# Performance work log

Measured on AMD Instinct MI355X. Metric: run time of the kernel, lower is better.

Reference implementation:

```python
import jax, jax.numpy as jnp
import numpy as np

N_NODES = 4096
JACOBI_ITERS = 10
EPS = 1e-5


def sym_laplacian_dense(edge_index, n):
    # L = I - D^{-1/2} A D^{-1/2}, duplicates in edge_index accumulate (as scipy COO does)
    row, col = edge_index[0], edge_index[1]
    A = jnp.zeros((n, n), jnp.float32).at[row, col].add(1.0)
    deg = A.sum(axis=1)
    dinv = jnp.where(deg > 0, 1.0 / jnp.sqrt(jnp.where(deg > 0, deg, 1.0)), 0.0)
    return jnp.eye(n, dtype=jnp.float32) - dinv[:, None] * A * dinv[None, :]


def jacobi_eig(a, iterations):
    # Faithful Jacobi: `iterations` Givens rotations, each zeroing the max |off-diag| entry.
    n = a.shape[0]
    upper = jnp.triu(jnp.ones((n, n), bool), k=1)

    def body(_, carry):
        a, p = carry
        idx = jnp.argmax(jnp.where(upper, jnp.abs(a), 0.0))
        k, l = idx // n, idx % n
        akl = a[k, l]
        aDiff = a[l, l] - a[k, k]
        akl_safe = jnp.where(akl == 0.0, 1.0, akl)
        aDiff_safe = jnp.where(aDiff == 0.0, 1.0, aDiff)
        phi = aDiff / (2.0 * akl_safe)
        t2 = 1.0 / (jnp.abs(phi) + jnp.sqrt(phi * phi + 1.0))
        t2 = jnp.where(phi < 0.0, -t2, t2)
        t1 = akl / aDiff_safe
        t = jnp.where(jnp.abs(akl) < jnp.abs(aDiff) * 1e-36, t1, t2)
        c = 1.0 / jnp.sqrt(t * t + 1.0)
        s = t * c
        # a <- G^T a G  (equivalent to the triangular in-place updates for symmetric a)
        ck, cl = a[:, k], a[:, l]
        a = a.at[:, k].set(c * ck - s * cl).at[:, l].set(s * ck + c * cl)
        rk, rl = a[k, :], a[l, :]
        a = a.at[k, :].set(c * rk - s * rl).at[l, :].set(s * rk + c * rl)
        a = a.at[k, l].set(0.0).at[l, k].set(0.0)
        pk, pl = p[:, k], p[:, l]
        p = p.at[:, k].set(c * pk - s * pl).at[:, l].set(s * pk + c * pl)
        return a, p

    a, p = jax.lax.fori_loop(0, iterations, body, (a, jnp.eye(n, dtype=a.dtype)))
    return jnp.diagonal(a), p


def setup_inputs() -> dict:
    key = jax.random.key(0)
    ks = jax.random.split(key, 8)
    n, cin, cout, r, e = N_NODES, 64, 64, 4, 100000
    x = jax.random.normal(ks[0], (n, cin), jnp.float32)
    src = jax.random.randint(ks[1], (e,), 0, n)
    dst = jax.random.randint(ks[2], (e,), 0, n)
    # symmetric graph (undirected), as the Jacobi solver assumes a symmetric Laplacian
    edge_index = jnp.stack([jnp.concatenate([src, dst]), jnp.concatenate([dst, src])]).astype(jnp.int64)
    stdv = 1.0 / np.sqrt(cin)
    real_weight = jax.random.uniform(ks[3], (cout, cin, r, 1), jnp.float32, -stdv, stdv)
    imag_weight = jax.random.uniform(ks[4], (cout, cin, r, 1), jnp.float32, -stdv, stdv)
    h = jax.random.uniform(ks[5], (cout, cin), jnp.float32, -stdv, stdv)
    c = jax.random.uniform(ks[6], (cout, cin, 1), jnp.float32, -stdv, stdv)
    bias = jnp.zeros((cout,), jnp.float32)
    return {"x": x, "edge_index": edge_index, "real_weight": real_weight,
            "imag_weight": imag_weight, "h": h, "c": c, "bias": bias}


def reference(x, edge_index, real_weight, imag_weight, h, c, bias):
    n = x.shape[0]
    r = real_weight.shape[2]
    L = sym_laplacian_dense(edge_index, n)
    w, U = jacobi_eig(L, JACOBI_ITERS)          # w: (N,), U: (N, N)
    aux = U.T @ x                                # (N, in)
    hw = h[:, :, None] * w[None, None, :]        # (out, in, N)
    a2 = jnp.where(hw > EPS,
                   2.0 * jnp.arctan(1.0 / jnp.where(hw > EPS, hw, 1.0)),
                   2.0)
    # theta[o,i,j,n] = a2[o,i,n] * (j+1)  -> (out, in, r, N)
    theta = a2[:, :, None, :] * jnp.arange(1, r + 1, dtype=x.dtype)[None, None, :, None]
    g = real_weight * jnp.cos(theta) - imag_weight * jnp.sin(theta)
    g = g.sum(axis=2) + c                        # (out, in, N)
    out = jnp.einsum('oin,ni->on', g, aux)       # Pmul + sum over in-channels
    output = U @ out.T + bias                    # (N, out); note: original's clamp(min=0) is a no-op
    return output
```

## Files before the change

kernel.cpp:

```cpp
#include <hip/hip_runtime.h>
#include <hip/hip_bf16.h>

#pragma clang fp contract(off)

#define N 4096
#define CIN 64
#define COUT 64
#define ITERS 10
#define MAXS 32
#define CANDMAX 384

typedef unsigned long long u64;

__device__ __forceinline__ u64 packkey(float v, unsigned j) {
    return ((u64)__float_as_uint(v) << 32) | (u64)(~j);
}
__device__ __forceinline__ u64 gkey(unsigned vb, unsigned row, unsigned col) {
    unsigned flat = (row << 12) | col;
    return ((u64)vb << 24) | (u64)((~flat) & 0xFFFFFFu);
}

__global__ void init_prep_k(int* __restrict__ deg, int* __restrict__ fill,
                            const float* __restrict__ hh, const float* __restrict__ cw,
                            const float* __restrict__ rw, const float* __restrict__ iw,
                            float2* __restrict__ hcT, float4* __restrict__ rwT,
                            float4* __restrict__ iwT) {
    int b = blockIdx.x;
    if (b < 16) {
        int i = b * 256 + threadIdx.x;
        deg[i] = 0; fill[i] = 0;
    } else {
        int idx = (b - 16) * 256 + threadIdx.x;
        int i = idx >> 6, o = idx & 63;
        int src = o * 64 + i;
        hcT[idx] = make_float2(hh[src], cw[src]);
        rwT[idx] = make_float4(rw[src * 4 + 0], rw[src * 4 + 1], rw[src * 4 + 2], rw[src * 4 + 3]);
        iwT[idx] = make_float4(iw[src * 4 + 0], iw[src * 4 + 1], iw[src * 4 + 2], iw[src * 4 + 3]);
    }
}

__global__ void edges1_k(const int* __restrict__ ei, int* __restrict__ deg, int E) {
    int e = blockIdx.x * 256 + threadIdx.x;
    if (e < E) atomicAdd(&deg[ei[e]], 1);
}

__global__ void __launch_bounds__(1024) scan_k(const int* __restrict__ deg,
                                               int* __restrict__ rowptr,
                                               float* __restrict__ dinv) {
    __shared__ int ps[1024];
    int t = threadIdx.x, b = t * 4;
    int d0 = deg[b], d1 = deg[b + 1], d2 = deg[b + 2], d3 = deg[b + 3];
    int local = d0 + d1 + d2 + d3;
    ps[t] = local;
    __syncthreads();
    for (int off = 1; off < 1024; off <<= 1) {
        int v = (t >= off) ? ps[t - off] : 0;
        __syncthreads();
        ps[t] += v;
        __syncthreads();
    }
    int excl = ps[t] - local;
    rowptr[b] = excl; rowptr[b + 1] = excl + d0;
    rowptr[b + 2] = excl + d0 + d1; rowptr[b + 3] = excl + d0 + d1 + d2;
    if (t == 1023) rowptr[4096] = ps[1023];
    dinv[b]     = d0 > 0 ? 1.0f / sqrtf((float)d0) : 0.0f;
    dinv[b + 1] = d1 > 0 ? 1.0f / sqrtf((float)d1) : 0.0f;
    dinv[b + 2] = d2 > 0 ? 1.0f / sqrtf((float)d2) : 0.0f;
    dinv[b + 3] = d3 > 0 ? 1.0f / sqrtf((float)d3) : 0.0f;
}

__global__ void edges2_k(const int* __restrict__ ei, const int* __restrict__ rowptr,
                         int* __restrict__ fill, int* __restrict__ colidx, int E) {
    int e = blockIdx.x * 256 + threadIdx.x;
    if (e < E) {
        int r = ei[e], c = ei[E + e];
        int pos = rowptr[r] + atomicAdd(&fill[r], 1);
        colidx[pos] = c;
    }
}

__global__ void __launch_bounds__(64) rowmax0_k(
        const int* __restrict__ rowptr, const int* __restrict__ colidx,
        const float* __restrict__ dinv, const float* __restrict__ x,
        float* __restrict__ y, float* __restrict__ diag, u64* __restrict__ top24T) {
    const int i = blockIdx.x, t = threadIdx.x;
    __shared__ float row[N];
    __shared__ u64 cand[CANDMAX];
    __shared__ int scnt;
    int rs = rowptr[i], re = rowptr[i + 1];
    if (t == 0) { scnt = 0; row[i] = 0.0f; }
    __syncthreads();
    for (int e = rs + t; e < re; e += 64) { int c2 = colidx[e]; if (c2 >= i) row[c2] = 0.0f; }
    __syncthreads();
    for (int e = rs + t; e < re; e += 64) { int c2 = colidx[e]; if (c2 >= i) atomicAdd(&row[c2], 1.0f); }
    __syncthreads();
    float di = dinv[i];
    for (int e = rs + t; e < re; e += 64) {
        int c2 = colidx[e];
        if (c2 > i) {
            float v = -((di * row[c2]) * dinv[c2]);
            int idx = atomicAdd(&scnt, 1);
            if (idx < CANDMAX) cand[idx] = packkey(fabsf(v), (unsigned)c2);
        }
    }
    __syncthreads();
    int L = scnt < CANDMAX ? scnt : CANDMAX;
    for (int r = 0; r < 24; ++r) {
        u64 best = 0ull;
        for (int idx = t; idx < L; idx += 64) { u64 cc = cand[idx]; if (cc > best) best = cc; }
        for (int off = 32; off; off >>= 1) { u64 o = __shfl_xor(best, off, 64); if (o > best) best = o; }
        if (t == 0) top24T[(size_t)r * N + i] = best;
        for (int idx = t; idx < L; idx += 64) { if (cand[idx] == best) cand[idx] = 0ull; }
        __syncthreads();
    }
    if (t == 0) diag[i] = 1.0f - ((di * row[i]) * di);
    y[i * CIN + t] = x[i * CIN + t];
}

__global__ void __launch_bounds__(1024) jacobi_k(
        const int* __restrict__ rowptr, const int* __restrict__ colidx,
        const float* __restrict__ dinv,
        float* __restrict__ diag, const u64* __restrict__ top24T, float* __restrict__ y,
        float* __restrict__ rowS, float* __restrict__ colS,
        int* __restrict__ dslotG, int* __restrict__ slistG, int* __restrict__ nslotsG,
        int* __restrict__ rotk, int* __restrict__ rotl,
        float* __restrict__ rotc, float* __restrict__ rotsv) {
    __shared__ float cntK[N], cntL[N];
    __shared__ u64 rmaxL[N];
    __shared__ float rvalL[N];
    __shared__ float diagL[N];
    __shared__ short dslotL[N];
    __shared__ u64 rmaxSlot[MAXS];
    __shared__ u64 w16[16], w16b[16];
    __shared__ float ovRowK[MAXS], ovRowL[MAXS], ovColK[MAXS], ovColL[MAXS];
    __shared__ int slistL[MAXS];
    __shared__ unsigned short sdirty[64];
    __shared__ int S_k, S_l, S_slotk, S_slotl, S_oldk, S_oldl, S_nold, S_ns, S_snd;
    __shared__ float S_c, S_s, S_a2kk, S_a2ll;
    __shared__ u64 S_pivot;
    const int t = threadIdx.x;

    u64 mb0 = 0ull;
    for (int i = t; i < N; i += 1024) {
        u64 kk = top24T[i];
        rmaxL[i] = kk;
        rvalL[i] = -__uint_as_float((unsigned)(kk >> 32));
        diagL[i] = diag[i];
        dslotL[i] = -1;
        unsigned col = (~(unsigned)kk) & 4095u;
        u64 gk = gkey((unsigned)(kk >> 32), (unsigned)i, col);
        if (gk > mb0) mb0 = gk;
    }
    if (t == 0) S_ns = 0;
    for (int off = 32; off; off >>= 1) { u64 o = __shfl_down(mb0, off, 64); if (o > mb0) mb0 = o; }
    if ((t & 63) == 0) w16[t >> 6] = mb0;
    __syncthreads();
    if (t == 0) { u64 b = w16[0]; for (int w = 1; w < 16; ++w) if (w16[w] > b) b = w16[w]; S_pivot = b; }
    __syncthreads();

    for (int it = 0; it < ITERS; ++it) {
        if (t == 0) {
            unsigned flat = (~(unsigned)S_pivot) & 0xFFFFFFu;
            int k = (int)(flat >> 12), l = (int)(flat & 4095u);
            float akl = rvalL[k];
            float akk = diagL[k], all_ = diagL[l];
            float aDiff = all_ - akk;
            float akl_safe = (akl == 0.0f) ? 1.0f : akl;
            float aDiff_safe = (aDiff == 0.0f) ? 1.0f : aDiff;
            float phi = aDiff / (2.0f * akl_safe);
            float t2 = 1.0f / (fabsf(phi) + sqrtf(phi * phi + 1.0f));
            t2 = (phi < 0.0f) ? -t2 : t2;
            float t1 = akl / aDiff_safe;
            float tt = (fabsf(akl) < fabsf(aDiff) * 1e-36f) ? t1 : t2;
            float cv = 1.0f / sqrtf(tt * tt + 1.0f);
            float sv = tt * cv;
            rotk[it] = k; rotl[it] = l; rotc[it] = cv; rotsv[it] = sv;
            float a1kk = cv * akk - sv * akl;
            float a1kl = sv * akk + cv * akl;
            float a1lk = cv * akl - sv * all_;
            float a1ll = sv * akl + cv * all_;
            S_a2kk = cv * a1kk - sv * a1lk;
            S_a2ll = sv * a1kl + cv * a1ll;
            diagL[k] = S_a2kk; diagL[l] = S_a2ll;
            int ns = S_ns;
            S_nold = ns;
            int ok = dslotL[k]; S_oldk = ok;
            int sk2 = ok; if (ok < 0) { sk2 = ns; slistL[ns] = k; dslotL[k] = (short)ns; ns++; }
            int ol = dslotL[l]; S_oldl = ol;
            int sl3 = ol; if (ol < 0) { sl3 = ns; slistL[ns] = l; dslotL[l] = (short)ns; ns++; }
            S_ns = ns;
            S_k = k; S_l = l; S_slotk = sk2; S_slotl = sl3; S_c = cv; S_s = sv;
            S_snd = 0;
        }
        __syncthreads();
        const int k = S_k, l = S_l, slotk = S_slotk, slotl = S_slotl;
        const int oldk = S_oldk, oldl = S_oldl, nold = S_nold, ns = S_ns;
        const float c = S_c, s = S_s;
        const float a2kk = S_a2kk, a2ll = S_a2ll;
        const bool freshK = (oldk < 0), freshL = (oldl < 0);
        const float dk = dinv[k], dl = dinv[l];
        if (t < CIN) {
            float yk = y[k * CIN + t], yl = y[l * CIN + t];
            y[k * CIN + t] = c * yk - s * yl;
            y[l * CIN + t] = s * yk + c * yl;
        }
        if (t >= 64 && t < 64 + nold) {
            int sl2 = t - 64;
            if (freshK) { ovRowK[sl2] = colS[(size_t)sl2 * N + k]; ovColK[sl2] = rowS[(size_t)sl2 * N + k]; }
            if (freshL) { ovRowL[sl2] = colS[(size_t)sl2 * N + l]; ovColL[sl2] = rowS[(size_t)sl2 * N + l]; }
        }
        if (freshK) for (int j = t; j < N; j += 1024) cntK[j] = 0.0f;
        if (freshL) for (int j = t; j < N; j += 1024) cntL[j] = 0.0f;
        __syncthreads();
        if (freshK || freshL) {
            if (freshK) for (int e = rowptr[k] + t; e < rowptr[k + 1]; e += 1024) atomicAdd(&cntK[colidx[e]], 1.0f);
            if (freshL) for (int e = rowptr[l] + t; e < rowptr[l + 1]; e += 1024) atomicAdd(&cntL[colidx[e]], 1.0f);
            __syncthreads();
        }
        u64 bk = packkey(0.0f, 4095u), bl = packkey(0.0f, 4095u);
        {
            const int j0 = t * 4;
            float4 dj4 = *reinterpret_cast<const float4*>(dinv + j0);
            float4 bK4, bL4, cK4, cL4;
            if (freshK) {
                float4 cnt = *reinterpret_cast<const float4*>(cntK + j0);
#pragma unroll
                for (int m = 0; m < 4; ++m) {
                    float cn = (&cnt.x)[m], dj = (&dj4.x)[m];
                    (&bK4.x)[m] = -((dk * cn) * dj);
                    (&cK4.x)[m] = -((dj * cn) * dk);
                }
            } else {
                bK4 = *reinterpret_cast<const float4*>(rowS + (size_t)oldk * N + j0);
                cK4 = *reinterpret_cast<const float4*>(colS + (size_t)oldk * N + j0);
            }
            if (freshL) {
                float4 cnt = *reinterpret_cast<const float4*>(cntL + j0);
#pragma unroll
                for (int m = 0; m < 4; ++m) {
                    float cn = (&cnt.x)[m], dj = (&dj4.x)[m];
                    (&bL4.x)[m] = -((dl * cn) * dj);
                    (&cL4.x)[m] = -((dj * cn) * dl);
                }
            } else {
                bL4 = *reinterpret_cast<const float4*>(rowS + (size_t)oldl * N + j0);
                cL4 = *reinterpret_cast<const float4*>(colS + (size_t)oldl * N + j0);
            }
            float4 nrK4, nrL4, ncK4, ncL4;
#pragma unroll
            for (int m = 0; m < 4; ++m) {
                int j = j0 + m;
                float bK = (&bK4.x)[m], bL = (&bL4.x)[m];
                float cK = (&cK4.x)[m], cL = (&cL4.x)[m];
                float nrk, nrl, nck, ncl;
                if (j == k)      { nrk = a2kk; nrl = 0.0f; nck = a2kk; ncl = 0.0f; }
                else if (j == l) { nrk = 0.0f; nrl = a2ll; nck = 0.0f; ncl = a2ll; }
                else {
                    int sl2 = dslotL[j];
                    if (sl2 >= 0 && sl2 < nold) {
                        if (freshK) { bK = ovRowK[sl2]; cK = ovColK[sl2]; }
                        if (freshL) { bL = ovRowL[sl2]; cL = ovColL[sl2]; }
                    }
                    nrk = c * bK - s * bL; nrl = s * bK + c * bL;
                    nck = c * cK - s * cL; ncl = s * cK + c * cL;
                }
                (&nrK4.x)[m] = nrk; (&nrL4.x)[m] = nrl;
                (&ncK4.x)[m] = nck; (&ncL4.x)[m] = ncl;
                if (j > k) { u64 kk = packkey(fabsf(nrk), (unsigned)j); if (kk > bk) bk = kk; }
                if (j > l) { u64 kk = packkey(fabsf(nrl), (unsigned)j); if (kk > bl) bl = kk; }
            }
            *reinterpret_cast<float4*>(rowS + (size_t)slotk * N + j0) = nrK4;
            *reinterpret_cast<float4*>(rowS + (size_t)slotl * N + j0) = nrL4;
            *reinterpret_cast<float4*>(colS + (size_t)slotk * N + j0) = ncK4;
            *reinterpret_cast<float4*>(colS + (size_t)slotl * N + j0) = ncL4;
            *reinterpret_cast<float4*>(cntK + j0) = ncK4;
            *reinterpret_cast<float4*>(cntL + j0) = ncL4;
        }
        for (int off = 32; off; off >>= 1) {
            u64 o = __shfl_down(bk, off, 64); if (o > bk) bk = o;
            u64 o2 = __shfl_down(bl, off, 64); if (o2 > bl) bl = o2;
        }
        if ((t & 63) == 0) { w16[t >> 6] = bk; w16b[t >> 6] = bl; }
        __syncthreads();
        if (t == 0) {
            u64 b1 = w16[0], b2 = w16b[0];
            for (int w = 1; w < 16; ++w) { if (w16[w] > b1) b1 = w16[w]; if (w16b[w] > b2) b2 = w16b[w]; }
            unsigned j1 = (~(unsigned)b1) & 4095u, j2 = (~(unsigned)b2) & 4095u;
            rvalL[k] = rowS[(size_t)slotk * N + j1];
            rvalL[l] = rowS[(size_t)slotl * N + j2];
            rmaxSlot[slotk] = gkey((unsigned)(b1 >> 32), (unsigned)k, j1);
            rmaxSlot[slotl] = gkey((unsigned)(b2 >> 32), (unsigned)l, j2);
        }
        if (t >= 64 && t < 64 + nold) {
            int sl2 = t - 64;
            int js = slistL[sl2];
            if (js != k && js != l) {
                float vkj = rowS[(size_t)slotk * N + js];
                float vlj = rowS[(size_t)slotl * N + js];
                float vjk = cntK[js];
                float vjl = cntL[js];
                colS[(size_t)sl2 * N + k] = vkj;
                colS[(size_t)sl2 * N + l] = vlj;
                rowS[(size_t)sl2 * N + k] = vjk;
                rowS[(size_t)sl2 * N + l] = vjl;
                u64 cached = rmaxSlot[sl2];
                unsigned cj = ((~(unsigned)cached) & 0xFFFFFFu) & 4095u;
                bool kc = (k > js), lc = (l > js);
                u64 ck2 = kc ? gkey(__float_as_uint(fabsf(vjk)), (unsigned)js, (unsigned)k) : 0ull;
                u64 cl2 = lc ? gkey(__float_as_uint(fabsf(vjl)), (unsigned)js, (unsigned)l) : 0ull;
                bool stale = false; u64 base = cached; bool useOld = true;
                if (kc && cj == (unsigned)k)      { if (ck2 < cached) stale = true; else { base = 0ull; useOld = false; } }
                else if (lc && cj == (unsigned)l) { if (cl2 < cached) stale = true; else { base = 0ull; useOld = false; } }
                if (!stale) {
                    if (kc || lc) {
                        u64 mm = base; float mv = useOld ? rvalL[js] : 0.0f;
                        if (ck2 > mm) { mm = ck2; mv = vjk; }
                        if (cl2 > mm) { mm = cl2; mv = vjl; }
                        rmaxSlot[sl2] = mm; rvalL[js] = mv;
                    }
                } else { int d2 = atomicAdd(&S_snd, 1); sdirty[d2] = (unsigned short)sl2; }
            }
        }
        u64 myBest = 0ull;
#pragma unroll
        for (int m = 0; m < 4; ++m) {
            int j = t + 1024 * m;
            if (j == k || j == l) continue;
            if (dslotL[j] >= 0) continue;
            float nck = cntK[j], ncl = cntL[j];
            u64 cached = rmaxL[j];
            unsigned cj = (~(unsigned)cached) & 4095u;
            bool kc = (k > j), lc = (l > j);
            u64 ck2 = kc ? packkey(fabsf(nck), (unsigned)k) : 0ull;
            u64 cl2 = lc ? packkey(fabsf(ncl), (unsigned)l) : 0ull;
            bool stale = false; u64 base = cached; bool useOld = true;
            if (kc && cj == (unsigned)k)      { if (ck2 < cached) stale = true; else { base = 0ull; useOld = false; } }
            else if (lc && cj == (unsigned)l) { if (cl2 < cached) stale = true; else { base = 0ull; useOld = false; } }
            if (!stale) {
                if (kc || lc) {
                    u64 mm = base; float mv = useOld ? rvalL[j] : 0.0f;
                    if (ck2 > mm) { mm = ck2; mv = nck; }
                    if (cl2 > mm) { mm = cl2; mv = ncl; }
                    rmaxL[j] = mm; rvalL[j] = mv;
                }
            } else {
                u64 bKey = 0ull; float bVal = 0.0f;
                for (int cc = 0; cc < 24; ++cc) {
                    u64 cand = top24T[(size_t)cc * N + j];
                    unsigned col = (~(unsigned)cand) & 4095u;
                    if (dslotL[col] < 0) {
                        bKey = cand;
                        bVal = -__uint_as_float((unsigned)(cand >> 32));
                        break;
                    }
                }
                for (int sl = 0; sl < ns; ++sl) {
                    if (sl == slotk || sl == slotl) continue;
                    int js = slistL[sl];
                    if (js > j) {
                        float v = colS[(size_t)sl * N + j];
                        u64 kk2 = packkey(fabsf(v), (unsigned)js);
                        if (kk2 > bKey) { bKey = kk2; bVal = v; }
                    }
                }
                if (kc && ck2 > bKey) { bKey = ck2; bVal = nck; }
                if (lc && cl2 > bKey) { bKey = cl2; bVal = ncl; }
                rmaxL[j] = bKey; rvalL[j] = bVal;
            }
            u64 fin = rmaxL[j];
            u64 gk = gkey((unsigned)(fin >> 32), (unsigned)j, (~(unsigned)fin) & 4095u);
            if (gk > myBest) myBest = gk;
        }
        __syncthreads();
        const int nd = S_snd;
        for (int d = 0; d < nd; ++d) {
            int sl2 = sdirty[d];
            int ir = slistL[sl2];
            u64 bb = packkey(0.0f, 4095u);
            int jb = t * 4;
            float4 v4 = *reinterpret_cast<const float4*>(rowS + (size_t)sl2 * N + jb);
#pragma unroll
            for (int m = 0; m < 4; ++m) {
                int j = jb + m;
                if (j > ir) {
                    u64 kk = packkey(fabsf((&v4.x)[m]), (unsigned)j);
                    if (kk > bb) bb = kk;
                }
            }
            for (int off = 32; off; off >>= 1) { u64 o = __shfl_down(bb, off, 64); if (o > bb) bb = o; }
            if ((t & 63) == 0) w16[t >> 6] = bb;
            __syncthreads();
            if (t == 0) {
                u64 b = w16[0];
                for (int w = 1; w < 16; ++w) if (w16[w] > b) b = w16[w];
                unsigned js2 = (~(unsigned)b) & 4095u;
                rmaxSlot[sl2] = gkey((unsigned)(b >> 32), (unsigned)ir, js2);
                rvalL[ir] = rowS[(size_t)sl2 * N + js2];
            }
            __syncthreads();
        }
        if (t < ns) { u64 o = rmaxSlot[t]; if (o > myBest) myBest = o; }
        for (int off = 32; off; off >>= 1) { u64 o = __shfl_down(myBest, off, 64); if (o > myBest) myBest = o; }
        if ((t & 63) == 0) w16[t >> 6] = myBest;
        __syncthreads();
        if (t == 0) { u64 b = w16[0]; for (int w = 1; w < 16; ++w) if (w16[w] > b) b = w16[w]; S_pivot = b; }
        __syncthreads();
    }
    for (int i = t; i < N; i += 1024) {
        diag[i] = diagL[i];
        dslotG[i] = (int)dslotL[i];
    }
    if (t < S_ns) slistG[t] = slistL[t];
    if (t == 0) *nslotsG = S_ns;
}

__global__ void __launch_bounds__(1024) spectral_k(
        const float* __restrict__ diag, const float* __restrict__ y,
        const float2* __restrict__ hcT, const float4* __restrict__ rwT,
        const float4* __restrict__ iwT, float* __restrict__ z) {
    int o = threadIdx.x & 63;
    int nl = threadIdx.x >> 6;
    int n = blockIdx.x * 16 + nl;
    __shared__ float saux[16][CIN];
    saux[nl][o] = y[n * CIN + o];
    __syncthreads();
    float wn = diag[n];
    const float C2 = -0.41614683654714241f;
    const float S2 = 0.90929742682568170f;
    float acc = 0.0f;
    for (int i = 0; i < CIN; ++i) {
        float2 hc = hcT[i * 64 + o];
        float hw = hc.x * wn;
        float t2v = hw * hw;
        float inv = 1.0f / (t2v + 1.0f);
        float c1 = (t2v - 1.0f) * inv;
        float s1 = (2.0f * hw) * inv;
        if (!(hw > 1e-5f)) { c1 = C2; s1 = S2; }
        float4 rwv = rwT[i * 64 + o];
        float4 iwv = iwT[i * 64 + o];
        float g = hc.y;
        float cj = c1, sj = s1;
        g += rwv.x * cj - iwv.x * sj;
        float cn = cj * c1 - sj * s1; float sn = sj * c1 + cj * s1; cj = cn; sj = sn;
        g += rwv.y * cj - iwv.y * sj;
        cn = cj * c1 - sj * s1; sn = sj * c1 + cj * s1; cj = cn; sj = sn;
        g += rwv.z * cj - iwv.z * sj;
        cn = cj * c1 - sj * s1; sn = sj * c1 + cj * s1; cj = cn; sj = sn;
        g += rwv.w * cj - iwv.w * sj;
        acc += g * saux[nl][i];
    }
    z[(size_t)n * COUT + o] = acc;
}

__global__ void store_fused_k(
        float* __restrict__ z, const float* __restrict__ bias,
        const int* __restrict__ dslot, const int* __restrict__ slistG,
        const int* __restrict__ nslotsG,
        const int* __restrict__ rotk, const int* __restrict__ rotl,
        const float* __restrict__ rotc, const float* __restrict__ rotsv,
        float* __restrict__ out) {
    int t = threadIdx.x;
    if (blockIdx.x < 1024) {
        int idx = blockIdx.x * 256 + t;
        int row = idx >> 6;
        if (dslot[row] < 0) out[idx] = z[idx] + bias[idx & 63];
    } else if (t < 64) {
        for (int i = ITERS - 1; i >= 0; --i) {
            int k = rotk[i], l = rotl[i];
            float c = rotc[i], s = rotsv[i];
            float zk = z[k * COUT + t];
            float zl = z[l * COUT + t];
            z[k * COUT + t] = c * zk + s * zl;
            z[l * COUT + t] = -s * zk + c * zl;
        }
        int ns = *nslotsG;
        for (int d = 0; d < ns; ++d) {
            int r = slistG[d];
            out[r * COUT + t] = z[r * COUT + t] + bias[t];
        }
    }
}

extern "C" void kernel_launch(void* const* d_in, const int* in_sizes, int n_in,
                              void* d_out, int out_size, void* d_ws, size_t ws_size,
                              hipStream_t stream) {
    const float* x   = (const float*)d_in[0];
    const int*   ei  = (const int*)d_in[1];
    const float* rw  = (const float*)d_in[2];
    const float* iw  = (const float*)d_in[3];
    const float* hh  = (const float*)d_in[4];
    const float* cw  = (const float*)d_in[5];
    const float* bias= (const float*)d_in[6];
    float* out = (float*)d_out;

    float* rowS = (float*)d_ws;
    float* colS = rowS + (size_t)MAXS * N;
    float* y    = colS + (size_t)MAXS * N;
    float* z    = y + N * CIN;
    float2* hcT = (float2*)(z + N * COUT);
    float4* rwT = (float4*)(hcT + 4096);
    float4* iwT = rwT + 4096;
    float* dinv = (float*)(iwT + 4096);
    float* diag = dinv + N;
    u64* top24T = (u64*)(diag + N);
    int* rowptr = (int*)(top24T + 24 * (size_t)N);
    int* fill   = rowptr + 4100;
    int* deg    = fill + N;
    int* slist  = deg + N;
    int* nslots = slist + 64;
    int* dslot  = nslots + 4;
    int* rotk   = dslot + N;
    int* rotl   = rotk + 16;
    float* rotc = (float*)(rotl + 16);
    float* rotsv= rotc + 16;
    int* colidx = (int*)(rotsv + 16);

    int E = in_sizes[1] / 2;
    int eb = (E + 255) / 256;

    init_prep_k<<<32, 256, 0, stream>>>(deg, fill, hh, cw, rw, iw, hcT, rwT, iwT);
    edges1_k<<<eb, 256, 0, stream>>>(ei, deg, E);
    scan_k<<<1, 1024, 0, stream>>>(deg, rowptr, dinv);
    edges2_k<<<eb, 256, 0, stream>>>(ei, rowptr, fill, colidx, E);
    rowmax0_k<<<N, 64, 0, stream>>>(rowptr, colidx, dinv, x, y, diag, top24T);

    jacobi_k<<<1, 1024, 0, stream>>>(rowptr, colidx, dinv, diag, top24T,
                                     y, rowS, colS, dslot, slist, nslots,
                                     rotk, rotl, rotc, rotsv);

    spectral_k<<<N / 16, 1024, 0, stream>>>(diag, y, hcT, rwT, iwT, z);
    store_fused_k<<<1025, 256, 0, stream>>>(z, bias, dslot, slist, nslots,
                                            rotk, rotl, rotc, rotsv, out);
}
```

Before: 264.1 us.

## Fuse spectral and store kernels, stage Jacobi rows in LDS, drop redundant syncs

Merges the spectral filter and the final store into one kernel. Rows touched by rotations are recomputed in a separate block and the inverse rotations are applied in shared memory, so the z buffer round trip through global memory goes away. The weight transpose moves into rowmax0_k, and the Jacobi loop now computes each rotation redundantly in every thread, which removes a barrier per iteration. Rotated rows and dinv are also kept in LDS instead of being read back from global memory. In exchange the kernel uses more shared memory, and one extra block recomputes the dirty rows serially.

```diff
diff --git a/kernel.cpp b/kernel.cpp
--- a/kernel.cpp
+++ b/kernel.cpp
@@ -20,23 +20,9 @@
     return ((u64)vb << 24) | (u64)((~flat) & 0xFFFFFFu);
 }
 
-__global__ void init_prep_k(int* __restrict__ deg, int* __restrict__ fill,
-                            const float* __restrict__ hh, const float* __restrict__ cw,
-                            const float* __restrict__ rw, const float* __restrict__ iw,
-                            float2* __restrict__ hcT, float4* __restrict__ rwT,
-                            float4* __restrict__ iwT) {
-    int b = blockIdx.x;
-    if (b < 16) {
-        int i = b * 256 + threadIdx.x;
-        deg[i] = 0; fill[i] = 0;
-    } else {
-        int idx = (b - 16) * 256 + threadIdx.x;
-        int i = idx >> 6, o = idx & 63;
-        int src = o * 64 + i;
-        hcT[idx] = make_float2(hh[src], cw[src]);
-        rwT[idx] = make_float4(rw[src * 4 + 0], rw[src * 4 + 1], rw[src * 4 + 2], rw[src * 4 + 3]);
-        iwT[idx] = make_float4(iw[src * 4 + 0], iw[src * 4 + 1], iw[src * 4 + 2], iw[src * 4 + 3]);
-    }
+__global__ void init_k(int* __restrict__ deg, int* __restrict__ fill) {
+    int i = blockIdx.x * 256 + threadIdx.x;
+    deg[i] = 0; fill[i] = 0;
 }
 
 __global__ void edges1_k(const int* __restrict__ ei, int* __restrict__ deg, int E) {
@@ -82,11 +68,21 @@
 __global__ void __launch_bounds__(64) rowmax0_k(
         const int* __restrict__ rowptr, const int* __restrict__ colidx,
         const float* __restrict__ dinv, const float* __restrict__ x,
-        float* __restrict__ y, float* __restrict__ diag, u64* __restrict__ top24T) {
+        float* __restrict__ y, float* __restrict__ diag, u64* __restrict__ top24T,
+        const float* __restrict__ hh, const float* __restrict__ cw,
+        const float* __restrict__ rw, const float* __restrict__ iw,
+        float2* __restrict__ hcT, float4* __restrict__ rwT, float4* __restrict__ iwT) {
     const int i = blockIdx.x, t = threadIdx.x;
     __shared__ float row[N];
     __shared__ u64 cand[CANDMAX];
     __shared__ int scnt;
+    if (t < 3) {
+        int ii = i >> 6, o = i & 63;
+        int src = o * 64 + ii;
+        if (t == 0) hcT[i] = make_float2(hh[src], cw[src]);
+        else if (t == 1) rwT[i] = make_float4(rw[src * 4 + 0], rw[src * 4 + 1], rw[src * 4 + 2], rw[src * 4 + 3]);
+        else iwT[i] = make_float4(iw[src * 4 + 0], iw[src * 4 + 1], iw[src * 4 + 2], iw[src * 4 + 3]);
+    }
     int rs = rowptr[i], re = rowptr[i + 1];
     if (t == 0) { scnt = 0; row[i] = 0.0f; }
     __syncthreads();
@@ -125,7 +121,9 @@
         int* __restrict__ dslotG, int* __restrict__ slistG, int* __restrict__ nslotsG,
         int* __restrict__ rotk, int* __restrict__ rotl,
         float* __restrict__ rotc, float* __restrict__ rotsv) {
-    __shared__ float cntK[N], cntL[N];
+    __shared__ __align__(16) float cntK[N], cntL[N];
+    __shared__ __align__(16) float rowKst[N], rowLst[N];
+    __shared__ __align__(16) float dinvL[N];
     __shared__ u64 rmaxL[N];
     __shared__ float rvalL[N];
     __shared__ float diagL[N];
@@ -135,9 +133,7 @@
     __shared__ float ovRowK[MAXS], ovRowL[MAXS], ovColK[MAXS], ovColL[MAXS];
     __shared__ int slistL[MAXS];
     __shared__ unsigned short sdirty[64];
-    __shared__ int S_k, S_l, S_slotk, S_slotl, S_oldk, S_oldl, S_nold, S_ns, S_snd;
-    __shared__ float S_c, S_s, S_a2kk, S_a2ll;
-    __shared__ u64 S_pivot;
+    __shared__ int S_snd;
     const int t = threadIdx.x;
 
     u64 mb0 = 0ull;
@@ -146,59 +142,57 @@
         rmaxL[i] = kk;
         rvalL[i] = -__uint_as_float((unsigned)(kk >> 32));
         diagL[i] = diag[i];
+        dinvL[i] = dinv[i];
         dslotL[i] = -1;
         unsigned col = (~(unsigned)kk) & 4095u;
         u64 gk = gkey((unsigned)(kk >> 32), (unsigned)i, col);
         if (gk > mb0) mb0 = gk;
     }
-    if (t == 0) S_ns = 0;
     for (int off = 32; off; off >>= 1) { u64 o = __shfl_down(mb0, off, 64); if (o > mb0) mb0 = o; }
     if ((t & 63) == 0) w16[t >> 6] = mb0;
     __syncthreads();
-    if (t == 0) { u64 b = w16[0]; for (int w = 1; w < 16; ++w) if (w16[w] > b) b = w16[w]; S_pivot = b; }
-    __syncthreads();
+    u64 pivot = w16[0];
+    for (int w = 1; w < 16; ++w) if (w16[w] > pivot) pivot = w16[w];
+    int nsCur = 0;
 
     for (int it = 0; it < ITERS; ++it) {
+        unsigned flat = (~(unsigned)pivot) & 0xFFFFFFu;
+        const int k = (int)(flat >> 12), l = (int)(flat & 4095u);
+        const float akl = rvalL[k];
+        const float akk = diagL[k], all_ = diagL[l];
+        float aDiff = all_ - akk;
+        float akl_safe = (akl == 0.0f) ? 1.0f : akl;
+        float aDiff_safe = (aDiff == 0.0f) ? 1.0f : aDiff;
+        float phi = aDiff / (2.0f * akl_safe);
+        float t2 = 1.0f / (fabsf(phi) + sqrtf(phi * phi + 1.0f));
+        t2 = (phi < 0.0f) ? -t2 : t2;
+        float t1 = akl / aDiff_safe;
+        float tt = (fabsf(akl) < fabsf(aDiff) * 1e-36f) ? t1 : t2;
+        const float c = 1.0f / sqrtf(tt * tt + 1.0f);
+        const float s = tt * c;
+        float a1kk = c * akk - s * akl;
+        float a1kl = s * akk + c * akl;
+        float a1lk = c * akl - s * all_;
+        float a1ll = s * akl + c * all_;
+        const float a2kk = c * a1kk - s * a1lk;
+        const float a2ll = s * a1kl + c * a1ll;
+        int ok = dslotL[k], ol = dslotL[l];
+        const int nold = nsCur;
+        const bool freshK = (ok < 0), freshL = (ol < 0);
+        int sk2 = ok, sl3 = ol;
+        { int ns = nsCur; if (freshK) sk2 = ns++; if (freshL) sl3 = ns++; nsCur = ns; }
+        const int slotk = sk2, slotl = sl3;
+        const float dk = dinvL[k], dl = dinvL[l];
+        if (freshK) for (int j = t; j < N; j += 1024) cntK[j] = 0.0f;
+        if (freshL) for (int j = t; j < N; j += 1024) cntL[j] = 0.0f;
+        __syncthreads();
         if (t == 0) {
-            unsigned flat = (~(unsigned)S_pivot) & 0xFFFFFFu;
-            int k = (int)(flat >> 12), l = (int)(flat & 4095u);
-            float akl = rvalL[k];
-            float akk = diagL[k], all_ = diagL[l];
-            float aDiff = all_ - akk;
-            float akl_safe = (akl == 0.0f) ? 1.0f : akl;
-            float aDiff_safe = (aDiff == 0.0f) ? 1.0f : aDiff;
-            float phi = aDiff / (2.0f * akl_safe);
-            float t2 = 1.0f / (fabsf(phi) + sqrtf(phi * phi + 1.0f));
-            t2 = (phi < 0.0f) ? -t2 : t2;
-            float t1 = akl / aDiff_safe;
-            float tt = (fabsf(akl) < fabsf(aDiff) * 1e-36f) ? t1 : t2;
-            float cv = 1.0f / sqrtf(tt * tt + 1.0f);
-            float sv = tt * cv;
-            rotk[it] = k; rotl[it] = l; rotc[it] = cv; rotsv[it] = sv;
-            float a1kk = cv * akk - sv * akl;
-            float a1kl = sv * akk + cv * akl;
-            float a1lk = cv * akl - sv * all_;
-            float a1ll = sv * akl + cv * all_;
-            S_a2kk = cv * a1kk - sv * a1lk;
-            S_a2ll = sv * a1kl + cv * a1ll;
-            diagL[k] = S_a2kk; diagL[l] = S_a2ll;
-            int ns = S_ns;
-            S_nold = ns;
-            int ok = dslotL[k]; S_oldk = ok;
-            int sk2 = ok; if (ok < 0) { sk2 = ns; slistL[ns] = k; dslotL[k] = (short)ns; ns++; }
-            int ol = dslotL[l]; S_oldl = ol;
-            int sl3 = ol; if (ol < 0) { sl3 = ns; slistL[ns] = l; dslotL[l] = (short)ns; ns++; }
-            S_ns = ns;
-            S_k = k; S_l = l; S_slotk = sk2; S_slotl = sl3; S_c = cv; S_s = sv;
+            rotk[it] = k; rotl[it] = l; rotc[it] = c; rotsv[it] = s;
+            diagL[k] = a2kk; diagL[l] = a2ll;
+            if (freshK) { slistL[slotk] = k; dslotL[k] = (short)slotk; }
+            if (freshL) { slistL[slotl] = l; dslotL[l] = (short)slotl; }
             S_snd = 0;
         }
-        __syncthreads();
-        const int k = S_k, l = S_l, slotk = S_slotk, slotl = S_slotl;
-        const int oldk = S_oldk, oldl = S_oldl, nold = S_nold, ns = S_ns;
-        const float c = S_c, s = S_s;
-        const float a2kk = S_a2kk, a2ll = S_a2ll;
-        const bool freshK = (oldk < 0), freshL = (oldl < 0);
-        const float dk = dinv[k], dl = dinv[l];
         if (t < CIN) {
             float yk = y[k * CIN + t], yl = y[l * CIN + t];
             y[k * CIN + t] = c * yk - s * yl;
@@ -209,18 +203,13 @@
             if (freshK) { ovRowK[sl2] = colS[(size_t)sl2 * N + k]; ovColK[sl2] = rowS[(size_t)sl2 * N + k]; }
             if (freshL) { ovRowL[sl2] = colS[(size_t)sl2 * N + l]; ovColL[sl2] = rowS[(size_t)sl2 * N + l]; }
         }
-        if (freshK) for (int j = t; j < N; j += 1024) cntK[j] = 0.0f;
-        if (freshL) for (int j = t; j < N; j += 1024) cntL[j] = 0.0f;
-        __syncthreads();
-        if (freshK || freshL) {
-            if (freshK) for (int e = rowptr[k] + t; e < rowptr[k + 1]; e += 1024) atomicAdd(&cntK[colidx[e]], 1.0f);
-            if (freshL) for (int e = rowptr[l] + t; e < rowptr[l + 1]; e += 1024) atomicAdd(&cntL[colidx[e]], 1.0f);
-            __syncthreads();
-        }
+        if (freshK) for (int e = rowptr[k] + t; e < rowptr[k + 1]; e += 1024) atomicAdd(&cntK[colidx[e]], 1.0f);
+        if (freshL) for (int e = rowptr[l] + t; e < rowptr[l + 1]; e += 1024) atomicAdd(&cntL[colidx[e]], 1.0f);
+        __syncthreads();
         u64 bk = packkey(0.0f, 4095u), bl = packkey(0.0f, 4095u);
         {
             const int j0 = t * 4;
-            float4 dj4 = *reinterpret_cast<const float4*>(dinv + j0);
+            float4 dj4 = *reinterpret_cast<const float4*>(dinvL + j0);
             float4 bK4, bL4, cK4, cL4;
             if (freshK) {
                 float4 cnt = *reinterpret_cast<const float4*>(cntK + j0);
@@ -231,8 +220,8 @@
                     (&cK4.x)[m] = -((dj * cn) * dk);
                 }
             } else {
-                bK4 = *reinterpret_cast<const float4*>(rowS + (size_t)oldk * N + j0);
-                cK4 = *reinterpret_cast<const float4*>(colS + (size_t)oldk * N + j0);
+                bK4 = *reinterpret_cast<const float4*>(rowS + (size_t)ok * N + j0);
+                cK4 = *reinterpret_cast<const float4*>(colS + (size_t)ok * N + j0);
             }
             if (freshL) {
                 float4 cnt = *reinterpret_cast<const float4*>(cntL + j0);
@@ -243,8 +232,8 @@
                     (&cL4.x)[m] = -((dj * cn) * dl);
                 }
             } else {
-                bL4 = *reinterpret_cast<const float4*>(rowS + (size_t)oldl * N + j0);
-                cL4 = *reinterpret_cast<const float4*>(colS + (size_t)oldl * N + j0);
+                bL4 = *reinterpret_cast<const float4*>(rowS + (size_t)ol * N + j0);
+                cL4 = *reinterpret_cast<const float4*>(colS + (size_t)ol * N + j0);
             }
             float4 nrK4, nrL4, ncK4, ncL4;
 #pragma unroll
@@ -273,6 +262,8 @@
             *reinterpret_cast<float4*>(rowS + (size_t)slotl * N + j0) = nrL4;
             *reinterpret_cast<float4*>(colS + (size_t)slotk * N + j0) = ncK4;
             *reinterpret_cast<float4*>(colS + (size_t)slotl * N + j0) = ncL4;
+            *reinterpret_cast<float4*>(rowKst + j0) = nrK4;
+            *reinterpret_cast<float4*>(rowLst + j0) = nrL4;
             *reinterpret_cast<float4*>(cntK + j0) = ncK4;
             *reinterpret_cast<float4*>(cntL + j0) = ncL4;
         }
@@ -286,8 +277,8 @@
             u64 b1 = w16[0], b2 = w16b[0];
             for (int w = 1; w < 16; ++w) { if (w16[w] > b1) b1 = w16[w]; if (w16b[w] > b2) b2 = w16b[w]; }
             unsigned j1 = (~(unsigned)b1) & 4095u, j2 = (~(unsigned)b2) & 4095u;
-            rvalL[k] = rowS[(size_t)slotk * N + j1];
-            rvalL[l] = rowS[(size_t)slotl * N + j2];
+            rvalL[k] = rowKst[j1];
+            rvalL[l] = rowLst[j2];
             rmaxSlot[slotk] = gkey((unsigned)(b1 >> 32), (unsigned)k, j1);
             rmaxSlot[slotl] = gkey((unsigned)(b2 >> 32), (unsigned)l, j2);
         }
@@ -295,8 +286,8 @@
             int sl2 = t - 64;
             int js = slistL[sl2];
             if (js != k && js != l) {
-                float vkj = rowS[(size_t)slotk * N + js];
-                float vlj = rowS[(size_t)slotl * N + js];
+                float vkj = rowKst[js];
+                float vlj = rowLst[js];
                 float vjk = cntK[js];
                 float vjl = cntL[js];
                 colS[(size_t)sl2 * N + k] = vkj;
@@ -325,7 +316,6 @@
 #pragma unroll
         for (int m = 0; m < 4; ++m) {
             int j = t + 1024 * m;
-            if (j == k || j == l) continue;
             if (dslotL[j] >= 0) continue;
             float nck = cntK[j], ncl = cntL[j];
             u64 cached = rmaxL[j];
@@ -354,7 +344,7 @@
                         break;
                     }
                 }
-                for (int sl = 0; sl < ns; ++sl) {
+                for (int sl = 0; sl < nsCur; ++sl) {
                     if (sl == slotk || sl == slotl) continue;
                     int js = slistL[sl];
                     if (js > j) {
@@ -399,84 +389,118 @@
             }
             __syncthreads();
         }
-        if (t < ns) { u64 o = rmaxSlot[t]; if (o > myBest) myBest = o; }
+        if (t < nsCur) { u64 o2 = rmaxSlot[t]; if (o2 > myBest) myBest = o2; }
         for (int off = 32; off; off >>= 1) { u64 o = __shfl_down(myBest, off, 64); if (o > myBest) myBest = o; }
         if ((t & 63) == 0) w16[t >> 6] = myBest;
         __syncthreads();
-        if (t == 0) { u64 b = w16[0]; for (int w = 1; w < 16; ++w) if (w16[w] > b) b = w16[w]; S_pivot = b; }
-        __syncthreads();
+        pivot = w16[0];
+        for (int w = 1; w < 16; ++w) if (w16[w] > pivot) pivot = w16[w];
     }
     for (int i = t; i < N; i += 1024) {
         diag[i] = diagL[i];
         dslotG[i] = (int)dslotL[i];
     }
-    if (t < S_ns) slistG[t] = slistL[t];
-    if (t == 0) *nslotsG = S_ns;
-}
-
-__global__ void __launch_bounds__(1024) spectral_k(
+    if (t < nsCur) slistG[t] = slistL[t];
+    if (t == 0) *nslotsG = nsCur;
+}
+
+__global__ void __launch_bounds__(1024) spectral_store_k(
         const float* __restrict__ diag, const float* __restrict__ y,
         const float2* __restrict__ hcT, const float4* __restrict__ rwT,
-        const float4* __restrict__ iwT, float* __restrict__ z) {
-    int o = threadIdx.x & 63;
-    int nl = threadIdx.x >> 6;
-    int n = blockIdx.x * 16 + nl;
-    __shared__ float saux[16][CIN];
-    saux[nl][o] = y[n * CIN + o];
-    __syncthreads();
-    float wn = diag[n];
-    const float C2 = -0.41614683654714241f;
-    const float S2 = 0.90929742682568170f;
-    float acc = 0.0f;
-    for (int i = 0; i < CIN; ++i) {
-        float2 hc = hcT[i * 64 + o];
-        float hw = hc.x * wn;
-        float t2v = hw * hw;
-        float inv = 1.0f / (t2v + 1.0f);
-        float c1 = (t2v - 1.0f) * inv;
-        float s1 = (2.0f * hw) * inv;
-        if (!(hw > 1e-5f)) { c1 = C2; s1 = S2; }
-        float4 rwv = rwT[i * 64 + o];
-        float4 iwv = iwT[i * 64 + o];
-        float g = hc.y;
-        float cj = c1, sj = s1;
-        g += rwv.x * cj - iwv.x * sj;
-        float cn = cj * c1 - sj * s1; float sn = sj * c1 + cj * s1; cj = cn; sj = sn;
-        g += rwv.y * cj - iwv.y * sj;
-        cn = cj * c1 - sj * s1; sn = sj * c1 + cj * s1; cj = cn; sj = sn;
-        g += rwv.z * cj - iwv.z * sj;
-        cn = cj * c1 - sj * s1; sn = sj * c1 + cj * s1; cj = cn; sj = sn;
-        g += rwv.w * cj - iwv.w * sj;
-        acc += g * saux[nl][i];
-    }
-    z[(size_t)n * COUT + o] = acc;
-}
-
-__global__ void store_fused_k(
-        float* __restrict__ z, const float* __restrict__ bias,
+        const float4* __restrict__ iwT, const float* __restrict__ bias,
         const int* __restrict__ dslot, const int* __restrict__ slistG,
         const int* __restrict__ nslotsG,
         const int* __restrict__ rotk, const int* __restrict__ rotl,
         const float* __restrict__ rotc, const float* __restrict__ rotsv,
         float* __restrict__ out) {
-    int t = threadIdx.x;
-    if (blockIdx.x < 1024) {
-        int idx = blockIdx.x * 256 + t;
-        int row = idx >> 6;
-        if (dslot[row] < 0) out[idx] = z[idx] + bias[idx & 63];
-    } else if (t < 64) {
-        for (int i = ITERS - 1; i >= 0; --i) {
-            int k = rotk[i], l = rotl[i];
-            float c = rotc[i], s = rotsv[i];
-            float zk = z[k * COUT + t];
-            float zl = z[l * COUT + t];
-            z[k * COUT + t] = c * zk + s * zl;
-            z[l * COUT + t] = -s * zk + c * zl;
-        }
+    __shared__ float saux[16][CIN];
+    __shared__ float2 shc[1024];
+    __shared__ float4 srw[1024];
+    __shared__ float4 siw[1024];
+    __shared__ float zloc[MAXS][COUT];
+    const int t = threadIdx.x;
+    const float C2 = -0.41614683654714241f;
+    const float S2 = 0.90929742682568170f;
+    if (blockIdx.x < 256) {
+        int o = t & 63, nl = t >> 6;
+        int n = blockIdx.x * 16 + nl;
+        saux[nl][o] = y[n * CIN + o];
+        float wn = diag[n];
+        float acc = 0.0f;
+        for (int ch = 0; ch < 4; ++ch) {
+            __syncthreads();
+            shc[t] = hcT[ch * 1024 + t];
+            srw[t] = rwT[ch * 1024 + t];
+            siw[t] = iwT[ch * 1024 + t];
+            __syncthreads();
+            for (int li = 0; li < 16; ++li) {
+                int i = ch * 16 + li;
+                float2 hc = shc[li * 64 + o];
+                float hw = hc.x * wn;
+                float t2v = hw * hw;
+                float inv = 1.0f / (t2v + 1.0f);
+                float c1 = (t2v - 1.0f) * inv;
+                float s1 = (2.0f * hw) * inv;
+                if (!(hw > 1e-5f)) { c1 = C2; s1 = S2; }
+                float4 rwv = srw[li * 64 + o];
+                float4 iwv = siw[li * 64 + o];
+                float g = hc.y;
+                float cj = c1, sj = s1;
+                g += rwv.x * cj - iwv.x * sj;
+                float cn = cj * c1 - sj * s1; float sn = sj * c1 + cj * s1; cj = cn; sj = sn;
+                g += rwv.y * cj - iwv.y * sj;
+                cn = cj * c1 - sj * s1; sn = sj * c1 + cj * s1; cj = cn; sj = sn;
+                g += rwv.z * cj - iwv.z * sj;
+                cn = cj * c1 - sj * s1; sn = sj * c1 + cj * s1; cj = cn; sj = sn;
+                g += rwv.w * cj - iwv.w * sj;
+                acc += g * saux[nl][i];
+            }
+        }
+        if (dslot[n] < 0) out[n * COUT + o] = acc + bias[o];
+    } else {
         int ns = *nslotsG;
-        for (int d = 0; d < ns; ++d) {
-            int r = slistG[d];
-            out[r * COUT + t] = z[r * COUT + t] + bias[t];
+        int o = t & 63, d = t >> 6;
+        for (int dd = d; dd < ns; dd += 16) {
+            int r = slistG[dd];
+            float wn = diag[r];
+            float acc = 0.0f;
+            for (int i = 0; i < CIN; ++i) {
+                float2 hc = hcT[i * 64 + o];
+                float hw = hc.x * wn;
+                float t2v = hw * hw;
+                float inv = 1.0f / (t2v + 1.0f);
+                float c1 = (t2v - 1.0f) * inv;
+                float s1 = (2.0f * hw) * inv;
+                if (!(hw > 1e-5f)) { c1 = C2; s1 = S2; }
+                float4 rwv = rwT[i * 64 + o];
+                float4 iwv = iwT[i * 64 + o];
+                float g = hc.y;
+                float cj = c1, sj = s1;
+                g += rwv.x * cj - iwv.x * sj;
+                float cn = cj * c1 - sj * s1; float sn = sj * c1 + cj * s1; cj = cn; sj = sn;
+                g += rwv.y * cj - iwv.y * sj;
+                cn = cj * c1 - sj * s1; sn = sj * c1 + cj * s1; cj = cn; sj = sn;
+                g += rwv.z * cj - iwv.z * sj;
+                cn = cj * c1 - sj * s1; sn = sj * c1 + cj * s1; cj = cn; sj = sn;
+                g += rwv.w * cj - iwv.w * sj;
+                acc += g * y[r * CIN + i];
+            }
+            zloc[dd][o] = acc;
+        }
+        __syncthreads();
+        if (t < 64) {
+            for (int i = ITERS - 1; i >= 0; --i) {
+                int k = rotk[i], l = rotl[i];
+                float c = rotc[i], s = rotsv[i];
+                int sk = dslot[k], sl = dslot[l];
+                float zk = zloc[sk][t], zl = zloc[sl][t];
+                zloc[sk][t] = c * zk + s * zl;
+                zloc[sl][t] = -s * zk + c * zl;
+            }
+        }
+        __syncthreads();
+        for (int dd = d; dd < ns; dd += 16) {
+            out[slistG[dd] * COUT + o] = zloc[dd][o] + bias[o];
         }
     }
 }
@@ -496,8 +520,7 @@
     float* rowS = (float*)d_ws;
     float* colS = rowS + (size_t)MAXS * N;
     float* y    = colS + (size_t)MAXS * N;
-    float* z    = y + N * CIN;
-    float2* hcT = (float2*)(z + N * COUT);
+    float2* hcT = (float2*)(y + N * CIN);
     float4* rwT = (float4*)(hcT + 4096);
     float4* iwT = rwT + 4096;
     float* dinv = (float*)(iwT + 4096);
@@ -518,17 +541,18 @@
     int E = in_sizes[1] / 2;
     int eb = (E + 255) / 256;
 
-    init_prep_k<<<32, 256, 0, stream>>>(deg, fill, hh, cw, rw, iw, hcT, rwT, iwT);
+    init_k<<<16, 256, 0, stream>>>(deg, fill);
     edges1_k<<<eb, 256, 0, stream>>>(ei, deg, E);
     scan_k<<<1, 1024, 0, stream>>>(deg, rowptr, dinv);
     edges2_k<<<eb, 256, 0, stream>>>(ei, rowptr, fill, colidx, E);
-    rowmax0_k<<<N, 64, 0, stream>>>(rowptr, colidx, dinv, x, y, diag, top24T);
+    rowmax0_k<<<N, 64, 0, stream>>>(rowptr, colidx, dinv, x, y, diag, top24T,
+                                    hh, cw, rw, iw, hcT, rwT, iwT);
 
     jacobi_k<<<1, 1024, 0, stream>>>(rowptr, colidx, dinv, diag, top24T,
                                      y, rowS, colS, dslot, slist, nslots,
                                      rotk, rotl, rotc, rotsv);
 
-    spectral_k<<<N / 16, 1024, 0, stream>>>(diag, y, hcT, rwT, iwT, z);
-    store_fused_k<<<1025, 256, 0, stream>>>(z, bias, dslot, slist, nslots,
-                                            rotk, rotl, rotc, rotsv, out);
-}
+    spectral_store_k<<<257, 1024, 0, stream>>>(diag, y, hcT, rwT, iwT, bias,
+                                               dslot, slist, nslots,
+                                               rotk, rotl, rotc, rotsv, out);
+}
```

Result: slower. 289.9 us (+9.8%).
